# Kernel optimization log

Measured on AMD Instinct MI355X. Metric: run time of the kernel, lower is better.

Reference implementation:

```python
import jax, jax.numpy as jnp
import numpy as np

B, L, F, H, HDE, E, V, MH, MW, TOUT = 64, 2, 512, 512, 512, 512, 94, 6, 40, 30
V2 = V + 2          # vocab + START/END + NULL slots
T = TOUT + 2        # decode steps
HW = MH * MW
START = V + 1
END = V + 1


def setup_inputs() -> dict:
    key = jax.random.key(0)
    ks = jax.random.split(key, 20)
    s = 0.05  # weight scale for numerical stability
    n = lambda k, shape: jax.random.normal(k, shape, jnp.float32) * s
    d = {}
    d['conv_f'] = jax.random.normal(ks[0], (B, F, MH, MW), jnp.float32)
    d['target'] = jax.random.randint(ks[1], (B, TOUT), 0, 95, dtype=jnp.int32)
    d['w_ih_en'] = n(ks[2], (L, 4 * H, F))
    d['w_hh_en'] = n(ks[3], (L, 4 * H, H))
    d['b_ih_en'] = n(ks[4], (L, 4 * H))
    d['b_hh_en'] = n(ks[5], (L, 4 * H))
    d['embed_w'] = n(ks[6], (V2, H))
    d['w_ih_de'] = n(ks[7], (L, 4 * HDE, H))
    d['w_hh_de'] = n(ks[8], (L, 4 * HDE, HDE))
    d['b_ih_de'] = n(ks[9], (L, 4 * HDE))
    d['b_hh_de'] = n(ks[10], (L, 4 * HDE))
    d['att_wh'] = n(ks[11], (E, HDE))
    d['att_bh'] = n(ks[12], (E,))
    d['att_conv_w'] = n(ks[13], (E, F, 3, 3))
    d['att_conv_b'] = n(ks[14], (E,))
    d['att_wv'] = n(ks[15], (1, E))
    d['att_bv'] = n(ks[16], (1,))
    d['out_w'] = n(ks[17], (V2, HDE + F))
    d['out_b'] = n(ks[18], (V2,))
    return d


def _lstm_cell(x, h, c, wih, whh, bih, bhh):
    # PyTorch gate order: i, f, g, o
    g = x @ wih.T + h @ whh.T + bih + bhh
    i, f, gg, o = jnp.split(g, 4, axis=-1)
    c_new = jax.nn.sigmoid(f) * c + jax.nn.sigmoid(i) * jnp.tanh(gg)
    h_new = jax.nn.sigmoid(o) * jnp.tanh(c_new)
    return h_new, c_new


def _forward(conv_f, target, w_ih_en, w_hh_en, b_ih_en, b_hh_en, embed_w,
             w_ih_de, w_hh_de, b_ih_de, b_hh_de, att_wh, att_bh,
             att_conv_w, att_conv_b, att_wv, att_bv, out_w, out_b):
    # ---- encoder: maxpool over full height, then 2-layer LSTM over width ----
    x_seq = jnp.max(conv_f, axis=2).transpose(2, 0, 1)  # [W, B, F]

    def enc_step(carry, xt):
        h, c = carry
        inp = xt
        hs, cs = [], []
        for l in range(L):
            hl, cl = _lstm_cell(inp, h[l], c[l], w_ih_en[l], w_hh_en[l],
                                b_ih_en[l], b_hh_en[l])
            inp = hl
            hs.append(hl); cs.append(cl)
        return (jnp.stack(hs), jnp.stack(cs)), inp

    z = jnp.zeros((L, B, H), conv_f.dtype)
    _, enc_out = jax.lax.scan(enc_step, (z, z), x_seq)
    holistic = enc_out[-1]  # [B, H]

    # ---- attention: conv_f embedding computed ONCE (invariant across steps) ----
    xe = jax.lax.conv_general_dilated(
        conv_f, att_conv_w, (1, 1), 'SAME',
        dimension_numbers=('NCHW', 'OIHW', 'NCHW')) + att_conv_b[None, :, None, None]
    x_em = xe.reshape(B, E, HW).transpose(0, 2, 1)       # [B, HW, E]
    cf_flat = conv_f.reshape(B, F, HW).transpose(0, 2, 1)  # [B, HW, F]

    # ---- decoder inputs: t=0 holistic, t>=1 embed(gt_with_start[:, t-1]) ----
    gt = jnp.concatenate(
        [jnp.full((B, 1), START, dtype=target.dtype), target], axis=1)  # [B, T-1]
    xs = jnp.concatenate([holistic[None], embed_w[gt.T]], axis=0)  # [T, B, H]

    def dec_step(carry, xt):
        h, c = carry
        inp = xt
        hs, cs = [], []
        for l in range(L):
            hl, cl = _lstm_cell(inp, h[l], c[l], w_ih_de[l], w_hh_de[l],
                                b_ih_de[l], b_hh_de[l])
            inp = hl
            hs.append(hl); cs.append(cl)
        hlast = inp  # [B, HDE]
        g_em = hlast @ att_wh.T + att_bh                    # [B, E]
        feat = jnp.tanh(x_em + g_em[:, None, :])            # [B, HW, E] (dropout=identity)
        e = feat @ att_wv[0] + att_bv[0]                    # [B, HW]
        alpha = jax.nn.softmax(e, axis=-1)
        att = jnp.einsum('bw,bwf->bf', alpha, cf_flat)      # [B, F]
        logits = jnp.concatenate([hlast, att], axis=-1) @ out_w.T + out_b
        scores = jax.nn.log_softmax(logits, axis=-1)        # [B, V2]
        return (jnp.stack(hs), jnp.stack(cs)), scores

    zd = jnp.zeros((B, HDE), conv_f.dtype)
    z0 = jnp.stack([zd] * L)
    _, out_tbv = jax.lax.scan(dec_step, (z0, z0), xs)  # [T, B, V2]
    out = out_tbv.transpose(1, 0, 2)                    # [B, T, V2]

    # ---- build l_target: [0, target..., 0] with first padding 0 -> END ----
    l_target = jnp.zeros((B, T), jnp.int32).at[:, 1:-1].set(target)
    j = jnp.argmax(l_target[:, 1:] == 0, axis=1) + 1  # first zero at col>=1 (always exists)
    l_target = l_target.at[jnp.arange(B), j].set(END)

    # ---- masked NLL loss ----
    lt = l_target.reshape(-1)
    nll = -out.reshape(-1, V2)[jnp.arange(B * T), lt]
    mask = (lt != 0).astype(out.dtype)
    return jnp.sum(nll * mask) / jnp.sum(mask)


def reference(conv_f, target, w_ih_en, w_hh_en, b_ih_en, b_hh_en, embed_w,
              w_ih_de, w_hh_de, b_ih_de, b_hh_de, att_wh, att_bh,
              att_conv_w, att_conv_b, att_wv, att_bv, out_w, out_b):
    return _forward(conv_f, target, w_ih_en, w_hh_en, b_ih_en, b_hh_en, embed_w,
                    w_ih_de, w_hh_de, b_ih_de, b_hh_de, att_wh, att_bh,
                    att_conv_w, att_conv_b, att_wv, att_bv, out_w, out_b)
```

## Files before the change

### kernel.cpp

```cpp
#include <hip/hip_runtime.h>

typedef __fp16 f16;
typedef __fp16 f16x4 __attribute__((ext_vector_type(4)));
typedef __fp16 f16x8 __attribute__((ext_vector_type(8)));
typedef float  f32x4 __attribute__((ext_vector_type(4)));
typedef unsigned long long ull;

#define DEV static __device__ __forceinline__

DEV f32x4 mfma16(f16x4 a, f16x4 b, f32x4 c) {
  return __builtin_amdgcn_mfma_f32_16x16x16f16(a, b, c, 0, 0, 0);
}
DEV f16x4 lo4(f16x8 v) { return __builtin_shufflevector(v, v, 0, 1, 2, 3); }
DEV f16x4 hi4(f16x8 v) { return __builtin_shufflevector(v, v, 4, 5, 6, 7); }
DEV float sigf(float x) { return 1.f / (1.f + __expf(-x)); }
DEV float tanh_(float x) { float e = __expf(2.f * x); return 1.f - 2.f / (e + 1.f); }

union U8 { float4 f4; float2 f2[2]; };
union H2 { unsigned u; f16 h[2]; };
union H4 { ull u; f16 h[4]; f16x4 v; };

#define HB 32768

DEV ull ldU(const ull* p) {
  return __hip_atomic_load(p, __ATOMIC_RELAXED, __HIP_MEMORY_SCOPE_AGENT);
}
DEV unsigned ldF(const unsigned* p) {
  return __hip_atomic_load(p, __ATOMIC_RELAXED, __HIP_MEMORY_SCOPE_AGENT);
}
DEV void stU32(unsigned* p, unsigned v) {
  __hip_atomic_store(p, v, __ATOMIC_RELAXED, __HIP_MEMORY_SCOPE_AGENT);
}
DEV void stU64(ull* p, ull v) {
  __hip_atomic_store(p, v, __ATOMIC_RELAXED, __HIP_MEMORY_SCOPE_AGENT);
}

DEV void wait8(const unsigned* line, unsigned tgt) {
  if (threadIdx.x < 8)
    while (ldF(line + threadIdx.x * 16) < tgt) {}
  __syncthreads();
}

DEV void signalDone(unsigned* line, int slot) {
  asm volatile("s_waitcnt vmcnt(0)" ::: "memory");
  __syncthreads();
  if (threadIdx.x == 0)
    __hip_atomic_fetch_add(line + slot * 16, 1u, __ATOMIC_RELAXED, __HIP_MEMORY_SCOPE_AGENT);
}

DEV void stageRow(const f16* __restrict__ s, f16* __restrict__ dstRow, int ch) {
  U8 u0, u1;
  u0.f4 = *(const float4*)s;
  u1.f4 = *(const float4*)(s + 8);
  *(float2*)(dstRow +  0 + ch * 4) = u0.f2[0];
  *(float2*)(dstRow + 16 + ch * 4) = u0.f2[1];
  *(float2*)(dstRow + 32 + ch * 4) = u1.f2[0];
  *(float2*)(dstRow + 48 + ch * 4) = u1.f2[1];
}

DEV void stageAu(const ull* __restrict__ srcU, f16 (*A)[64][72], int tid) {
  int row = tid >> 2, ch = tid & 3;
  const ull* s = srcU + row * 128 + ch * 4;
#pragma unroll
  for (int c = 0; c < 8; ++c) {
    ull d0 = ldU(s + c * 16 + 0);
    ull d1 = ldU(s + c * 16 + 1);
    ull d2 = ldU(s + c * 16 + 2);
    ull d3 = ldU(s + c * 16 + 3);
    f16* d = &A[c][row][0];
    *(ull*)(d +  0 + ch * 4) = d0;
    *(ull*)(d + 16 + ch * 4) = d1;
    *(ull*)(d + 32 + ch * 4) = d2;
    *(ull*)(d + 48 + ch * 4) = d3;
  }
}

DEV void kloop32(const f16 (*Wt)[32][72], const f16 (*A)[64][72],
                 int mh, int ns, int m16, int g4, f32x4 acc[2]) {
#pragma unroll
  for (int c = 0; c < 8; ++c) {
#pragma unroll
    for (int half = 0; half < 2; ++half) {
      f16x8 bf = *(const f16x8*)&Wt[c][ns * 16 + m16][g4 * 16 + half * 8];
      f16x4 bl = lo4(bf), bh = hi4(bf);
#pragma unroll
      for (int mt = 0; mt < 2; ++mt) {
        f16x8 af = *(const f16x8*)&A[c][mh * 32 + mt * 16 + m16][g4 * 16 + half * 8];
        acc[mt] = mfma16(lo4(af), bl, acc[mt]);
        acc[mt] = mfma16(hi4(af), bh, acc[mt]);
      }
    }
  }
}

DEV void kloop64(const f16* Wg, const f16 (*A)[64][72],
                 int nsG, int m16, int g4, f32x4 acc[4]) {
#pragma unroll
  for (int c = 0; c < 8; ++c) {
#pragma unroll
    for (int half = 0; half < 2; ++half) {
      f16x8 bf = *(const f16x8*)&Wg[((size_t)(c * 64 + nsG * 16 + m16)) * 72 + g4 * 16 + half * 8];
      f16x4 bl = lo4(bf), bh = hi4(bf);
#pragma unroll
      for (int mt = 0; mt < 4; ++mt) {
        f16x8 af = *(const f16x8*)&A[c][mt * 16 + m16][g4 * 16 + half * 8];
        acc[mt] = mfma16(lo4(af), bl, acc[mt]);
        acc[mt] = mfma16(hi4(af), bh, acc[mt]);
      }
    }
  }
}

DEV void convTile(char* smem, int tile, const f16* __restrict__ cfT,
                  const f16* __restrict__ wc9, const float* __restrict__ cb,
                  f16* __restrict__ xemH) {
  f16 (*At)[40] = (f16(*)[40])smem;
  f16 (*Bt)[40] = (f16(*)[40])(smem + 19200);
  const int t = threadIdx.x, lane = t & 63, w = t >> 6;
  const int b = tile >> 2, eb = (tile & 3) * 128;
  const int m16 = lane & 15, g4 = lane >> 4;
  f32x4 acc[15][2] = {};

  for (int kr = 0; kr < 9; ++kr) {
    int dh = kr / 3 - 1, dw = kr % 3 - 1;
    for (int f0 = 0; f0 < 512; f0 += 32) {
      __syncthreads();
      if (t < 240) {
        int hh = t / 40 + dh, ww = t % 40 + dw;
        if (hh >= 0 && hh < 6 && ww >= 0 && ww < 40) {
          const f16* s = cfT + ((size_t)(b * 240 + hh * 40 + ww) * 512 + f0);
          U8 u0, u1, u2, u3;
          u0.f4 = *(const float4*)s;        u1.f4 = *(const float4*)(s + 8);
          u2.f4 = *(const float4*)(s + 16); u3.f4 = *(const float4*)(s + 24);
          *(float2*)&At[t][ 0] = u0.f2[0];
          *(float2*)&At[t][ 8] = u0.f2[1];
          *(float2*)&At[t][16] = u1.f2[0];
          *(float2*)&At[t][24] = u1.f2[1];
          *(float2*)&At[t][ 4] = u2.f2[0];
          *(float2*)&At[t][12] = u2.f2[1];
          *(float2*)&At[t][20] = u3.f2[0];
          *(float2*)&At[t][28] = u3.f2[1];
        } else {
          float2 z = make_float2(0.f, 0.f);
          *(float2*)&At[t][ 0] = z; *(float2*)&At[t][ 8] = z;
          *(float2*)&At[t][16] = z; *(float2*)&At[t][24] = z;
          *(float2*)&At[t][ 4] = z; *(float2*)&At[t][12] = z;
          *(float2*)&At[t][20] = z; *(float2*)&At[t][28] = z;
        }
      }
      {
        int n = t >> 1, ch = t & 1;
        const f16* s = wc9 + (size_t)(eb + n) * 4608 + kr * 512 + f0 + ch * 16;
        U8 u0, u1;
        u0.f4 = *(const float4*)s; u1.f4 = *(const float4*)(s + 8);
        *(float2*)&Bt[n][ 0 + ch * 4] = u0.f2[0];
        *(float2*)&Bt[n][ 8 + ch * 4] = u0.f2[1];
        *(float2*)&Bt[n][16 + ch * 4] = u1.f2[0];
        *(float2*)&Bt[n][24 + ch * 4] = u1.f2[1];
      }
      __syncthreads();
      f16x8 b0 = *(const f16x8*)&Bt[w * 32 + m16][g4 * 8];
      f16x8 b1v = *(const f16x8*)&Bt[w * 32 + 16 + m16][g4 * 8];
      f16x4 b0l = lo4(b0), b0h = hi4(b0), b1l = lo4(b1v), b1h = hi4(b1v);
#pragma unroll
      for (int mt = 0; mt < 15; ++mt) {
        f16x8 af = *(const f16x8*)&At[mt * 16 + m16][g4 * 8];
        f16x4 al = lo4(af), ah = hi4(af);
        acc[mt][0] = mfma16(al, b0l, acc[mt][0]);
        acc[mt][1] = mfma16(al, b1l, acc[mt][1]);
        acc[mt][0] = mfma16(ah, b0h, acc[mt][0]);
        acc[mt][1] = mfma16(ah, b1h, acc[mt][1]);
      }
    }
  }
#pragma unroll
  for (int nt = 0; nt < 2; ++nt) {
    int e = eb + w * 32 + nt * 16 + m16;
    float bias = cb[e];
#pragma unroll
    for (int mt = 0; mt < 15; ++mt)
#pragma unroll
      for (int r = 0; r < 4; ++r) {
        int p = mt * 16 + g4 * 4 + r;
        xemH[((size_t)(b * 240 + p)) * 512 + e] = (f16)(acc[mt][nt][r] + bias);
      }
  }
}


__global__ void k_convW(const float* __restrict__ s0, const float* __restrict__ s1,
                        const float* __restrict__ s2, const float* __restrict__ s3,
                        f16* __restrict__ d0, f16* __restrict__ d1,
                        f16* __restrict__ d2, f16* __restrict__ d3) {
  int i = blockIdx.x * 256 + threadIdx.x;
  int sel = i >> 19, j = i & 524287;
  const float* s = sel == 0 ? s0 : sel == 1 ? s1 : sel == 2 ? s2 : s3;
  f16* d = sel == 0 ? d0 : sel == 1 ? d1 : sel == 2 ? d2 : d3;
  float4 v = ((const float4*)s)[j];
  f16x4 o = { (f16)v.x, (f16)v.y, (f16)v.z, (f16)v.w };
  *(f16x4*)(d + (size_t)j * 4) = o;
}

__global__ void k_convS(const float* __restrict__ awhS, const float* __restrict__ embS,
                        const float* __restrict__ outwS,
                        f16* __restrict__ awhD, f16* __restrict__ embD,
                        f16* __restrict__ outwD) {
  int i = blockIdx.x * 256 + threadIdx.x;
  const float* s; f16* d; int j;
  if (i < 65536) { s = awhS; d = awhD; j = i; }
  else if (i < 65536 + 12288) { s = embS; d = embD; j = i - 65536; }
  else if (i < 65536 + 12288 + 24576) { s = outwS; d = outwD; j = i - 65536 - 12288; }
  else return;
  float4 v = ((const float4*)s)[j];
  f16x4 o = { (f16)v.x, (f16)v.y, (f16)v.z, (f16)v.w };
  *(f16x4*)(d + (size_t)j * 4) = o;
}

__global__ __launch_bounds__(256) void k_wc9(const float* __restrict__ src, f16* __restrict__ dst) {
  __shared__ float s[4608];
  const int e = blockIdx.x, tid = threadIdx.x;
  for (int i = tid; i < 4608; i += 256) s[i] = src[(size_t)e * 4608 + i];
  __syncthreads();
  for (int j = tid; j < 4608; j += 256) {
    int rr = j >> 9, f = j & 511;
    dst[(size_t)e * 4608 + j] = (f16)s[f * 9 + rr];
  }
}

__global__ __launch_bounds__(256) void k_cfmx(
    const float* __restrict__ cf, f16* __restrict__ cfT, f16* __restrict__ xseq)
{
  __shared__ float sT[64][244];
  const int tid = threadIdx.x;
  const int f0 = blockIdx.x * 64, b = blockIdx.y;
  const float* src = cf + ((size_t)b * 512 + f0) * 240;
  for (int i = tid; i < 3840; i += 256) {
    float4 v = ((const float4*)src)[i];
    int fl = i / 60, pc = (i % 60) * 4;
    sT[fl][pc] = v.x; sT[fl][pc + 1] = v.y; sT[fl][pc + 2] = v.z; sT[fl][pc + 3] = v.w;
  }
  __syncthreads();
  if (tid < 240) {
    int p = tid;
    f16* drow = cfT + ((size_t)b * 240 + p) * 512 + f0;
#pragma unroll
    for (int j = 0; j < 8; ++j) {
      f16x8 o;
#pragma unroll
      for (int k = 0; k < 8; ++k) o[k] = (f16)sT[j * 8 + k][p];
      *(f16x8*)(drow + j * 8) = o;
    }
  }
  {
    int fl = tid >> 2, wq = tid & 3;
#pragma unroll
    for (int wi = 0; wi < 10; ++wi) {
      int w = wq * 10 + wi;
      float m = sT[fl][w];
#pragma unroll
      for (int h = 1; h < 6; ++h) m = fmaxf(m, sT[fl][h * 40 + w]);
      xseq[((size_t)w * 64 + b) * 512 + f0 + fl] = (f16)m;
    }
  }
}

__global__ void k_zero(unsigned* p0, unsigned* p1, unsigned* p2,
                       unsigned* p3, unsigned* p4, unsigned* p5) {
  int i = blockIdx.x * 256 + threadIdx.x;
  int sel = i >> 14, j = i & 16383;
  unsigned* p = sel == 0 ? p0 : sel == 1 ? p1 : sel == 2 ? p2 :
                sel == 3 ? p3 : sel == 4 ? p4 : p5;
  p[j] = 0;
}

__global__ __launch_bounds__(256) void k_gemmX(
    const f16* __restrict__ A, const f16* __restrict__ W,
    const float* __restrict__ b1, const float* __restrict__ b2,
    f16* __restrict__ C)
{
  __shared__ f16 At[64][72];
  __shared__ f16 Bt[64][72];
  const int t = threadIdx.x, lane = t & 63, g = t >> 6;
  f32x4 acc[4] = {};
  const int m16 = lane & 15, g4 = lane >> 4;
  const size_t arow0 = (size_t)blockIdx.x * 64;

  for (int k0 = 0; k0 < 512; k0 += 64) {
    __syncthreads();
    { int row = t >> 2, ch = t & 3;
      stageRow(A + (arow0 + row) * 512 + k0 + ch * 16, &At[row][0], ch); }
    { int row = t >> 2, ch = t & 3;
      stageRow(W + ((size_t)blockIdx.y * 64 + row) * 512 + k0 + ch * 16, &Bt[row][0], ch); }
    __syncthreads();
#pragma unroll
    for (int half = 0; half < 2; ++half) {
      f16x8 bf = *(const f16x8*)&Bt[g * 16 + m16][g4 * 16 + half * 8];
      f16x4 bl = lo4(bf), bh = hi4(bf);
#pragma unroll
      for (int mt = 0; mt < 4; ++mt) {
        f16x8 af = *(const f16x8*)&At[mt * 16 + m16][g4 * 16 + half * 8];
        acc[mt] = mfma16(lo4(af), bl, acc[mt]);
        acc[mt] = mfma16(hi4(af), bh, acc[mt]);
      }
    }
  }
  int e = blockIdx.y * 64 + g * 16 + m16;
  float bias = b1[e] + b2[e];
#pragma unroll
  for (int mt = 0; mt < 4; ++mt)
#pragma unroll
    for (int r = 0; r < 4; ++r)
      C[(arow0 + mt * 16 + g4 * 4 + r) * 2048 + e] = (f16)(acc[mt][r] + bias);
}

__global__ __launch_bounds__(256) void k_gemmXd(
    const f16* __restrict__ x_t0, const f16* __restrict__ emb, const int* __restrict__ tgt,
    const f16* __restrict__ W, const float* __restrict__ b1, const float* __restrict__ b2,
    f16* __restrict__ C)
{
  __shared__ f16 At[64][72];
  __shared__ f16 Bt[64][72];
  const int t = threadIdx.x, lane = t & 63, g = t >> 6;
  f32x4 acc[4] = {};
  const int m16 = lane & 15, g4 = lane >> 4;
  const int tt = blockIdx.x;
  const size_t arow0 = (size_t)tt * 64;
  const int row = t >> 2, ch = t & 3;
  const f16* rowSrc;
  if (tt == 0) rowSrc = x_t0 + (size_t)row * 512;
  else if (tt == 1) rowSrc = emb + (size_t)95 * 512;
  else { int tok = tgt[row * 30 + tt - 2]; rowSrc = emb + (size_t)tok * 512; }

  for (int k0 = 0; k0 < 512; k0 += 64) {
    __syncthreads();
    stageRow(rowSrc + k0 + ch * 16, &At[row][0], ch);
    stageRow(W + ((size_t)blockIdx.y * 64 + row) * 512 + k0 + ch * 16, &Bt[row][0], ch);
    __syncthreads();
#pragma unroll
    for (int half = 0; half < 2; ++half) {
      f16x8 bf = *(const f16x8*)&Bt[g * 16 + m16][g4 * 16 + half * 8];
      f16x4 bl = lo4(bf), bh = hi4(bf);
#pragma unroll
      for (int mt = 0; mt < 4; ++mt) {
        f16x8 af = *(const f16x8*)&At[mt * 16 + m16][g4 * 16 + half * 8];
        acc[mt] = mfma16(lo4(af), bl, acc[mt]);
        acc[mt] = mfma16(hi4(af), bh, acc[mt]);
      }
    }
  }
  int e = blockIdx.y * 64 + g * 16 + m16;
  float bias = b1[e] + b2[e];
#pragma unroll
  for (int mt = 0; mt < 4; ++mt)
#pragma unroll
    for (int r = 0; r < 4; ++r)
      C[(arow0 + mt * 16 + g4 * 4 + r) * 2048 + e] = (f16)(acc[mt][r] + bias);
}

__global__ __launch_bounds__(256) void k_gemmG(
    const f16* __restrict__ A, const f16* __restrict__ W,
    const float* __restrict__ b1, f16* __restrict__ C)
{
  __shared__ f16 At[64][72];
  __shared__ f16 Bt[64][72];
  const int t = threadIdx.x, lane = t & 63, g = t >> 6;
  f32x4 acc[4] = {};
  const int m16 = lane & 15, g4 = lane >> 4;
  const size_t arow0 = (size_t)blockIdx.x * 64;

  for (int k0 = 0; k0 < 512; k0 += 64) {
    __syncthreads();
    { int row = t >> 2, ch = t & 3;
      stageRow(A + (arow0 + row) * 512 + k0 + ch * 16, &At[row][0], ch); }
    { int row = t >> 2, ch = t & 3;
      stageRow(W + ((size_t)blockIdx.y * 64 + row) * 512 + k0 + ch * 16, &Bt[row][0], ch); }
    __syncthreads();
#pragma unroll
    for (int half = 0; half < 2; ++half) {
      f16x8 bf = *(const f16x8*)&Bt[g * 16 + m16][g4 * 16 + half * 8];
      f16x4 bl = lo4(bf), bh = hi4(bf);
#pragma unroll
      for (int mt = 0; mt < 4; ++mt) {
        f16x8 af = *(const f16x8*)&At[mt * 16 + m16][g4 * 16 + half * 8];
        acc[mt] = mfma16(lo4(af), bl, acc[mt]);
        acc[mt] = mfma16(hi4(af), bh, acc[mt]);
      }
    }
  }
  int e = blockIdx.y * 64 + g * 16 + m16;
  float bias = b1[e];
#pragma unroll
  for (int mt = 0; mt < 4; ++mt)
#pragma unroll
    for (int r = 0; r < 4; ++r)
      C[(arow0 + mt * 16 + g4 * 4 + r) * 512 + e] = (f16)(acc[mt][r] + bias);
}

__global__ __launch_bounds__(256, 1) void k_lstm(
    int T,
    const f16* __restrict__ G0, const f16* __restrict__ whh0,
    const f16* __restrict__ wih1, const f16* __restrict__ whh1,
    const float* __restrict__ bih1, const float* __restrict__ bhh1,
    f16* __restrict__ h0seq, f16* __restrict__ h1seq,
    unsigned* __restrict__ cnt,
    const f16* __restrict__ cfT, const f16* __restrict__ wc9,
    const float* __restrict__ cb, f16* __restrict__ xemH, int convBase)
{
  __shared__ __align__(16) char smem[147456];
  const int tid = threadIdx.x, lane = tid & 63, w = tid >> 6;
  const int m16 = lane & 15, g4 = lane >> 4;
  const int bid = blockIdx.x;

  if (bid >= 96) {
    convTile(smem, convBase + bid - 96, cfT, wc9, cb, xemH);
    return;
  }

  if (bid < 32) {
    f16 (*sW)[64][72] = (f16(*)[64][72])smem;
    f16 (*sA)[64][72] = (f16(*)[64][72])(smem + 73728);
    float* sG = (float*)(smem + 73728);
    const int utile = bid;
    { int r = tid >> 2, ch = tid & 3;
      int grow = (r >> 4) * 512 + utile * 16 + (r & 15);
      for (int c = 0; c < 8; ++c)
        stageRow(whh0 + (size_t)grow * 512 + c * 64 + ch * 16, &sW[c][r][0], ch);
    }
    const int pb = tid >> 2, uq = tid & 3;
    float cst[4] = {0.f, 0.f, 0.f, 0.f};
    for (int t = 0; t < T; ++t) {
      if (t > 0) wait8(cnt + (size_t)(t - 1) * 128, 4);
      const f16* gpp = G0 + (size_t)(t * 64 + pb) * 2048 + utile * 16 + uq * 4;
      H4 gI, gF, gG, gO;
      gI.v = *(const f16x4*)(gpp);
      gF.v = *(const f16x4*)(gpp + 512);
      gG.v = *(const f16x4*)(gpp + 1024);
      gO.v = *(const f16x4*)(gpp + 1536);
      stageAu((const ull*)h0seq + (size_t)t * 8192, sA, tid);
      __syncthreads();
      f32x4 acc[4] = {};
      kloop64((const f16*)sW, sA, w, m16, g4, acc);
      __syncthreads();
#pragma unroll
      for (int mt = 0; mt < 4; ++mt)
#pragma unroll
        for (int r = 0; r < 4; ++r)
          sG[((size_t)w * 64 + mt * 16 + g4 * 4 + r) * 17 + m16] = acc[mt][r];
      __syncthreads();
      {
        H4 outp;
#pragma unroll
        for (int j = 0; j < 4; ++j) {
          int u = uq * 4 + j;
          float gi = sG[(0 * 64 + pb) * 17 + u] + (float)gI.h[j];
          float gf = sG[(1 * 64 + pb) * 17 + u] + (float)gF.h[j];
          float gg = sG[(2 * 64 + pb) * 17 + u] + (float)gG.h[j];
          float go = sG[(3 * 64 + pb) * 17 + u] + (float)gO.h[j];
          float cn = sigf(gf) * cst[j] + sigf(gi) * tanh_(gg);
          float hn = sigf(go) * tanh_(cn);
          cst[j] = cn;
          outp.h[j] = (f16)hn;
        }
        stU64((ull*)h0seq + (size_t)(t + 1) * 8192 + pb * 128 + utile * 4 + uq, outp.u);
      }
      signalDone(cnt + (size_t)t * 128, bid & 7);
    }
  } else {
    f16 (*sW2)[8][32][72] = (f16(*)[8][32][72])smem;
    f16 (*sA)[64][72] = (f16(*)[64][72])(smem + 73728);
    float* sG = (float*)(smem + 73728);
    const int utile = bid - 32;
    const int mh = w >> 1, ns = w & 1;
    { int mat = tid >> 7;
      int r = (tid >> 2) & 31, ch = tid & 3;
      int grow = (r >> 3) * 512 + utile * 8 + (r & 7);
      const f16* Wsrc = (mat == 0) ? wih1 : whh1;
      for (int c = 0; c < 8; ++c)
        stageRow(Wsrc + (size_t)grow * 512 + c * 64 + ch * 16, &sW2[mat][c][r][0], ch);
    }
    const int pb = tid >> 2, pup = tid & 3;
    float badd[4][2];
#pragma unroll
    for (int g = 0; g < 4; ++g)
#pragma unroll
      for (int j = 0; j < 2; ++j) {
        int rr = g * 512 + utile * 8 + pup * 2 + j;
        badd[g][j] = bih1[rr] + bhh1[rr];
      }
    float cst[2] = {0.f, 0.f};
    unsigned* line1 = cnt + (size_t)T * 128;
    for (int t = 0; t < T; ++t) {
      wait8(cnt + (size_t)t * 128, 4);
      stageAu((const ull*)h0seq + (size_t)(t + 1) * 8192, sA, tid);
      if (t > 0) wait8(line1 + (size_t)(t - 1) * 128, 8);
      else       __syncthreads();
      ull rg[8][4];
      { const ull* s1p = (const ull*)h1seq + (size_t)t * 8192 + (tid >> 2) * 128 + (tid & 3) * 4;
#pragma unroll
        for (int c = 0; c < 8; ++c)
#pragma unroll
          for (int q = 0; q < 4; ++q) rg[c][q] = ldU(s1p + c * 16 + q);
      }
      f32x4 acc[2] = {};
      kloop32(sW2[0], sA, mh, ns, m16, g4, acc);
      __syncthreads();
      { int row = tid >> 2, ch = tid & 3;
#pragma unroll
        for (int c = 0; c < 8; ++c) {
          f16* d = &sA[c][row][0];
          *(ull*)(d +  0 + ch * 4) = rg[c][0];
          *(ull*)(d + 16 + ch * 4) = rg[c][1];
          *(ull*)(d + 32 + ch * 4) = rg[c][2];
          *(ull*)(d + 48 + ch * 4) = rg[c][3];
        }
      }
      __syncthreads();
      kloop32(sW2[1], sA, mh, ns, m16, g4, acc);
      __syncthreads();
      { int nl = ns * 16 + m16;
#pragma unroll
        for (int mt = 0; mt < 2; ++mt)
#pragma unroll
          for (int r = 0; r < 4; ++r) {
            int b = mh * 32 + mt * 16 + g4 * 4 + r;
            sG[((nl >> 3) * 64 + b) * 9 + (nl & 7)] = acc[mt][r];
          }
      }
      __syncthreads();
      {
        H2 outp;
#pragma unroll
        for (int j = 0; j < 2; ++j) {
          int u = pup * 2 + j;
          float gi = sG[(0 * 64 + pb) * 9 + u] + badd[0][j];
          float gf = sG[(1 * 64 + pb) * 9 + u] + badd[1][j];
          float gg = sG[(2 * 64 + pb) * 9 + u] + badd[2][j];
          float go = sG[(3 * 64 + pb) * 9 + u] + badd[3][j];
          float cn = sigf(gf) * cst[j] + sigf(gi) * tanh_(gg);
          float hn = sigf(go) * tanh_(cn);
          cst[j] = cn;
          outp.h[j] = (f16)hn;
        }
        stU32((unsigned*)h1seq + (size_t)(t + 1) * 16384 + pb * 256 + utile * 4 + pup, outp.u);
      }
      signalDone(line1 + (size_t)t * 128, bid & 7);
    }
  }
}


__global__ __launch_bounds__(256) void k_scoreAll(
    const f16* __restrict__ xemH, const f16* __restrict__ gAll,
    const float* __restrict__ wv, float* __restrict__ esc)
{
  __shared__ f16 sX[20][512];
  const int tid = threadIdx.x, lane = tid & 63, w = tid >> 6;
  const int tile = blockIdx.x, b = blockIdx.y;
  for (int i = tid; i < 20 * 64; i += 256) {
    int row = i >> 6, seg = i & 63;
    *(f16x8*)&sX[row][seg * 8] =
        *(const f16x8*)(xemH + ((size_t)(b * 240 + tile * 20 + row)) * 512 + seg * 8);
  }
  float w8[8];
  { const float4* wp = (const float4*)(wv + lane * 8);
    float4 wa = wp[0], wb = wp[1];
    w8[0] = wa.x; w8[1] = wa.y; w8[2] = wa.z; w8[3] = wa.w;
    w8[4] = wb.x; w8[5] = wb.y; w8[6] = wb.z; w8[7] = wb.w; }
  __syncthreads();
  for (int t = 0; t < 32; ++t) {
    f16x8 gv = *(const f16x8*)(gAll + ((size_t)(t * 64 + b)) * 512 + lane * 8);
    float g8[8];
#pragma unroll
    for (int j = 0; j < 8; ++j) g8[j] = (float)gv[j];
#pragma unroll
    for (int i = 0; i < 5; ++i) {
      int rr = i * 4 + w;
      f16x8 xv = *(const f16x8*)&sX[rr][lane * 8];
      float s = 0.f;
#pragma unroll
      for (int j = 0; j < 8; ++j) s += tanh_((float)xv[j] + g8[j]) * w8[j];
#pragma unroll
      for (int m = 32; m; m >>= 1) s += __shfl_xor(s, m);
      if (lane == 0) esc[((size_t)(t * 64 + b)) * 240 + tile * 20 + rr] = s;
    }
  }
}

__global__ __launch_bounds__(256) void k_smctx(
    const float* __restrict__ esc, const f16* __restrict__ cfT,
    const f16* __restrict__ h1seq, f16* __restrict__ ctx)
{
  __shared__ float aAl[8][240];
  const int tid = threadIdx.x, lane = tid & 63, w = tid >> 6;
  const int tq = blockIdx.x, b = blockIdx.y;
  for (int half = 0; half < 2; ++half) {
    int tt = w + half * 4;
    int t = tq * 8 + tt;
    const float* er = esc + ((size_t)(t * 64 + b)) * 240;
    float v[4];
    float mx = -1e30f;
#pragma unroll
    for (int q = 0; q < 4; ++q) {
      int p = lane + q * 64;
      v[q] = (p < 240) ? er[p] : -1e30f;
      mx = fmaxf(mx, v[q]);
    }
#pragma unroll
    for (int m = 32; m; m >>= 1) mx = fmaxf(mx, __shfl_xor(mx, m));
    float sum = 0.f;
#pragma unroll
    for (int q = 0; q < 4; ++q) { v[q] = __expf(v[q] - mx); sum += v[q]; }
#pragma unroll
    for (int m = 32; m; m >>= 1) sum += __shfl_xor(sum, m);
    float inv = 1.f / sum;
#pragma unroll
    for (int q = 0; q < 4; ++q) {
      int p = lane + q * 64;
      if (p < 240) aAl[tt][p] = v[q] * inv;
    }
  }
  __syncthreads();
  float acc[8][2] = {};
  const f16* cb = cfT + (size_t)b * 240 * 512;
  for (int p = 0; p < 240; ++p) {
    H2 cw; cw.u = *(const unsigned*)(cb + (size_t)p * 512 + tid * 2);
    float c0 = (float)cw.h[0], c1 = (float)cw.h[1];
#pragma unroll
    for (int tt = 0; tt < 8; ++tt) {
      float a = aAl[tt][p];
      acc[tt][0] += a * c0;
      acc[tt][1] += a * c1;
    }
  }
#pragma unroll
  for (int tt = 0; tt < 8; ++tt) {
    int t = tq * 8 + tt;
    size_t r = (size_t)(t * 64 + b);
    H2 o; o.h[0] = (f16)acc[tt][0]; o.h[1] = (f16)acc[tt][1];
    *(unsigned*)(ctx + r * 1024 + 512 + tid * 2) = o.u;
    *(unsigned*)(ctx + r * 1024 + tid * 2) =
        *(const unsigned*)(h1seq + (size_t)(t + 1) * HB + b * 512 + tid * 2);
  }
}

__global__ __launch_bounds__(256) void k_gemmL(
    const f16* __restrict__ A, const f16* __restrict__ W,
    const float* __restrict__ bias, float* __restrict__ C)
{
  __shared__ f16 At[64][72];
  __shared__ f16 Bt[64][72];
  const int t = threadIdx.x, lane = t & 63, g = t >> 6;
  f32x4 acc[4] = {};
  const int m16 = lane & 15, g4 = lane >> 4;
  const size_t arow0 = (size_t)blockIdx.x * 64;

  for (int k0 = 0; k0 < 1024; k0 += 64) {
    __syncthreads();
    { int row = t >> 2, ch = t & 3;
      stageRow(A + (arow0 + row) * 1024 + k0 + ch * 16, &At[row][0], ch); }
    { int row = t >> 2, ch = t & 3;
      stageRow(W + ((size_t)(blockIdx.y * 64 + row)) * 1024 + k0 + ch * 16, &Bt[row][0], ch); }
    __syncthreads();
#pragma unroll
    for (int half = 0; half < 2; ++half) {
      f16x8 bf = *(const f16x8*)&Bt[g * 16 + m16][g4 * 16 + half * 8];
      f16x4 bl = lo4(bf), bh = hi4(bf);
#pragma unroll
      for (int mt = 0; mt < 4; ++mt) {
        f16x8 af = *(const f16x8*)&At[mt * 16 + m16][g4 * 16 + half * 8];
        acc[mt] = mfma16(lo4(af), bl, acc[mt]);
        acc[mt] = mfma16(hi4(af), bh, acc[mt]);
      }
    }
  }
  int e = blockIdx.y * 64 + g * 16 + m16;
  if (e < 96) {
    float be = bias[e];
#pragma unroll
    for (int mt = 0; mt < 4; ++mt)
#pragma unroll
      for (int r = 0; r < 4; ++r)
        C[(arow0 + mt * 16 + g4 * 4 + r) * 96 + e] = acc[mt][r] + be;
  }
}

__global__ void k_nllloss(const float* __restrict__ lgt, const int* __restrict__ target,
                          float* __restrict__ out) {
  __shared__ int ltg[2048];
  __shared__ float sa[256], sb[256];
  int tid = threadIdx.x;
  if (tid < 64) {
    int b = tid;
    int row[32];
    row[0] = 0;
    for (int t = 1; t <= 30; ++t) row[t] = target[b * 30 + t - 1];
    row[31] = 0;
    int j = 1;
    while (row[j] != 0) ++j;
    row[j] = 95;
    for (int t = 0; t < 32; ++t) ltg[b * 32 + t] = row[t];
  }
  __syncthreads();
  float a = 0.f, m = 0.f;
  for (int r = tid; r < 2048; r += 256) {
    int t = r >> 6, b = r & 63;
    int tok = ltg[b * 32 + t];
    if (tok != 0) {
      const float* row = lgt + (size_t)r * 96;
      float mx = -1e30f;
      for (int j = 0; j < 96; ++j) mx = fmaxf(mx, row[j]);
      float s = 0.f;
      for (int j = 0; j < 96; ++j) s += __expf(row[j] - mx);
      a += mx + __logf(s) - row[tok];
      m += 1.f;
    }
  }
  sa[tid] = a; sb[tid] = m; __syncthreads();
  for (int s = 128; s; s >>= 1) { if (tid < s) { sa[tid] += sa[tid + s]; sb[tid] += sb[tid + s]; } __syncthreads(); }
  if (tid == 0) out[0] = sa[0] / sb[0];
}


extern "C" void kernel_launch(void* const* d_in, const int* in_sizes, int n_in,
                              void* d_out, int out_size, void* d_ws, size_t ws_size,
                              hipStream_t stream) {
  (void)in_sizes; (void)n_in; (void)out_size; (void)ws_size;
  const float* conv_f = (const float*)d_in[0];
  const int*   target = (const int*)d_in[1];
  const float* wih_en = (const float*)d_in[2];
  const float* whh_en = (const float*)d_in[3];
  const float* bih_en = (const float*)d_in[4];
  const float* bhh_en = (const float*)d_in[5];
  const float* embed  = (const float*)d_in[6];
  const float* wih_de = (const float*)d_in[7];
  const float* whh_de = (const float*)d_in[8];
  const float* bih_de = (const float*)d_in[9];
  const float* bhh_de = (const float*)d_in[10];
  const float* att_wh = (const float*)d_in[11];
  const float* att_bh = (const float*)d_in[12];
  const float* att_cw = (const float*)d_in[13];
  const float* att_cb = (const float*)d_in[14];
  const float* att_wv = (const float*)d_in[15];
  const float* out_w  = (const float*)d_in[17];
  const float* out_b  = (const float*)d_in[18];
  float* out = (float*)d_out;

  size_t o = 0;
  char* base = (char*)d_ws;
  auto take = [&](size_t bytes) -> void* {
    void* p = base + o;
    o += (bytes + 255) & ~(size_t)255;
    return p;
  };
  const size_t WSZ = (size_t)2048 * 512;
  f16* wihEn = (f16*)take(2 * WSZ * 2);
  f16* whhEn = (f16*)take(2 * WSZ * 2);
  f16* wihDe = (f16*)take(2 * WSZ * 2);
  f16* whhDe = (f16*)take(2 * WSZ * 2);
  f16* awh   = (f16*)take((size_t)512 * 512 * 2);
  f16* emb   = (f16*)take((size_t)96 * 512 * 2);
  f16* wc9   = (f16*)take((size_t)512 * 4608 * 2);
  f16* cfT   = (f16*)take((size_t)64 * 240 * 512 * 2);
  f16* xseq  = (f16*)take((size_t)40 * 64 * 512 * 2);
  f16* xemH  = (f16*)take((size_t)64 * 240 * 512 * 2);
  f16* outwH = (f16*)take((size_t)128 * 1024 * 2);
  f16* X0en  = (f16*)take((size_t)2560 * 2048 * 2);
  f16* X0de  = (f16*)take((size_t)2048 * 2048 * 2);
  f16* h0seqE = (f16*)take((size_t)41 * HB * 2);
  f16* h1seqE = (f16*)take((size_t)41 * HB * 2);
  f16* h0seqD = (f16*)take((size_t)33 * HB * 2);
  f16* h1seqD = (f16*)take((size_t)33 * HB * 2);
  f16* gAll   = (f16*)take((size_t)2048 * 512 * 2);
  unsigned* cntE = (unsigned*)take(65536);
  unsigned* cntD = (unsigned*)take(65536);
  float* escAll = (float*)X0en;
  float* lgtAll = (float*)((char*)X0en + 4194304);
  f16*   ctxAll = X0de;

  k_convW<<<8192, 256, 0, stream>>>(wih_en, whh_en, wih_de, whh_de,
                                    wihEn, whhEn, wihDe, whhDe);
  k_convS<<<400, 256, 0, stream>>>(att_wh, embed, out_w, awh, emb, outwH);
  k_wc9<<<512, 256, 0, stream>>>(att_cw, wc9);
  k_cfmx<<<dim3(8, 64), 256, 0, stream>>>(conv_f, cfT, xseq);
  k_zero<<<384, 256, 0, stream>>>((unsigned*)h0seqE, (unsigned*)h1seqE,
                                  (unsigned*)h0seqD, (unsigned*)h1seqD, cntE, cntD);

  k_gemmX<<<dim3(40, 32), 256, 0, stream>>>(xseq, wihEn, bih_en, bhh_en, X0en);
  k_lstm<<<224, 256, 0, stream>>>(40, X0en, whhEn, wihEn + WSZ, whhEn + WSZ,
                                  bih_en + 2048, bhh_en + 2048, h0seqE, h1seqE, cntE,
                                  cfT, wc9, att_cb, xemH, 0);

  k_gemmXd<<<dim3(32, 32), 256, 0, stream>>>(h1seqE + (size_t)40 * HB, emb, target,
                                             wihDe, bih_de, bhh_de, X0de);
  k_lstm<<<224, 256, 0, stream>>>(32, X0de, whhDe, wihDe + WSZ, whhDe + WSZ,
                                  bih_de + 2048, bhh_de + 2048, h0seqD, h1seqD, cntD,
                                  cfT, wc9, att_cb, xemH, 128);

  k_gemmG<<<dim3(32, 8), 256, 0, stream>>>(h1seqD + HB, awh, att_bh, gAll);
  k_scoreAll<<<dim3(12, 64), 256, 0, stream>>>(xemH, gAll, att_wv, escAll);
  k_smctx<<<dim3(4, 64), 256, 0, stream>>>(escAll, cfT, h1seqD, ctxAll);
  k_gemmL<<<dim3(32, 2), 256, 0, stream>>>(ctxAll, outwH, out_b, lgtAll);
  k_nllloss<<<1, 256, 0, stream>>>(lgtAll, target, out);
}
```

Before: 856.4 us.

## Fold decoder input GEMM and attention projection GEMM into persistent LSTM kernels

The encoder LSTM launch gains 32 extra blocks that compute the decoder layer-0 input projection for steps 1..31 from the embeddings while the encoder recurrence runs. The separate decoder input GEMM is cut down to the one step that depends on the final encoder state. The decoder LSTM launch gains 8 blocks that poll the layer-1 step counters and compute the attention hidden projection (gAll) per step as each h1 becomes ready, replacing the separate k_gemmG launch. This overlaps otherwise serial GEMMs with the latency-bound recurrence, but it adds co-resident blocks that spin-wait and assumes all 256 or 232 blocks are resident at once.

```diff
diff --git a/kernel.cpp b/kernel.cpp
--- a/kernel.cpp
+++ b/kernel.cpp
@@ -56,6 +56,14 @@
   *(float2*)(dstRow + 16 + ch * 4) = u0.f2[1];
   *(float2*)(dstRow + 32 + ch * 4) = u1.f2[0];
   *(float2*)(dstRow + 48 + ch * 4) = u1.f2[1];
+}
+
+DEV void stageAp(const f16* __restrict__ rowSrc, f16 (*A)[64][72], int tid) {
+  int ch = tid & 3;
+  const f16* s = rowSrc + ch * 16;
+#pragma unroll
+  for (int c = 0; c < 8; ++c)
+    stageRow(s + c * 64, &A[c][tid >> 2][0], ch);
 }
 
 DEV void stageAu(const ull* __restrict__ srcU, f16 (*A)[64][72], int tid) {
@@ -357,64 +365,24 @@
       C[(arow0 + mt * 16 + g4 * 4 + r) * 2048 + e] = (f16)(acc[mt][r] + bias);
 }
 
-__global__ __launch_bounds__(256) void k_gemmG(
-    const f16* __restrict__ A, const f16* __restrict__ W,
-    const float* __restrict__ b1, f16* __restrict__ C)
-{
-  __shared__ f16 At[64][72];
-  __shared__ f16 Bt[64][72];
-  const int t = threadIdx.x, lane = t & 63, g = t >> 6;
-  f32x4 acc[4] = {};
-  const int m16 = lane & 15, g4 = lane >> 4;
-  const size_t arow0 = (size_t)blockIdx.x * 64;
-
-  for (int k0 = 0; k0 < 512; k0 += 64) {
-    __syncthreads();
-    { int row = t >> 2, ch = t & 3;
-      stageRow(A + (arow0 + row) * 512 + k0 + ch * 16, &At[row][0], ch); }
-    { int row = t >> 2, ch = t & 3;
-      stageRow(W + ((size_t)blockIdx.y * 64 + row) * 512 + k0 + ch * 16, &Bt[row][0], ch); }
-    __syncthreads();
-#pragma unroll
-    for (int half = 0; half < 2; ++half) {
-      f16x8 bf = *(const f16x8*)&Bt[g * 16 + m16][g4 * 16 + half * 8];
-      f16x4 bl = lo4(bf), bh = hi4(bf);
-#pragma unroll
-      for (int mt = 0; mt < 4; ++mt) {
-        f16x8 af = *(const f16x8*)&At[mt * 16 + m16][g4 * 16 + half * 8];
-        acc[mt] = mfma16(lo4(af), bl, acc[mt]);
-        acc[mt] = mfma16(hi4(af), bh, acc[mt]);
-      }
-    }
-  }
-  int e = blockIdx.y * 64 + g * 16 + m16;
-  float bias = b1[e];
-#pragma unroll
-  for (int mt = 0; mt < 4; ++mt)
-#pragma unroll
-    for (int r = 0; r < 4; ++r)
-      C[(arow0 + mt * 16 + g4 * 4 + r) * 512 + e] = (f16)(acc[mt][r] + bias);
-}
-
 __global__ __launch_bounds__(256, 1) void k_lstm(
-    int T,
+    int T, int mode,
     const f16* __restrict__ G0, const f16* __restrict__ whh0,
     const f16* __restrict__ wih1, const f16* __restrict__ whh1,
     const float* __restrict__ bih1, const float* __restrict__ bhh1,
     f16* __restrict__ h0seq, f16* __restrict__ h1seq,
     unsigned* __restrict__ cnt,
     const f16* __restrict__ cfT, const f16* __restrict__ wc9,
-    const float* __restrict__ cb, f16* __restrict__ xemH, int convBase)
+    const float* __restrict__ cb, f16* __restrict__ xemH, int convBase,
+    f16* __restrict__ X0de, const f16* __restrict__ wihD0,
+    const float* __restrict__ bihD0, const float* __restrict__ bhhD0,
+    const f16* __restrict__ emb, const int* __restrict__ tgt,
+    const f16* __restrict__ awh, const float* __restrict__ gbias, f16* __restrict__ gAll)
 {
   __shared__ __align__(16) char smem[147456];
   const int tid = threadIdx.x, lane = tid & 63, w = tid >> 6;
   const int m16 = lane & 15, g4 = lane >> 4;
   const int bid = blockIdx.x;
-
-  if (bid >= 96) {
-    convTile(smem, convBase + bid - 96, cfT, wc9, cb, xemH);
-    return;
-  }
 
   if (bid < 32) {
     f16 (*sW)[64][72] = (f16(*)[64][72])smem;
@@ -465,7 +433,7 @@
       }
       signalDone(cnt + (size_t)t * 128, bid & 7);
     }
-  } else {
+  } else if (bid < 96) {
     f16 (*sW2)[8][32][72] = (f16(*)[8][32][72])smem;
     f16 (*sA)[64][72] = (f16(*)[64][72])(smem + 73728);
     float* sG = (float*)(smem + 73728);
@@ -544,6 +512,61 @@
         stU32((unsigned*)h1seq + (size_t)(t + 1) * 16384 + pb * 256 + utile * 4 + pup, outp.u);
       }
       signalDone(line1 + (size_t)t * 128, bid & 7);
+    }
+  } else if (bid < 224) {
+    convTile(smem, convBase + bid - 96, cfT, wc9, cb, xemH);
+  } else if (mode == 0) {
+    const int rid = bid - 224;
+    f16 (*sW)[64][72] = (f16(*)[64][72])smem;
+    f16 (*sA)[64][72] = (f16(*)[64][72])(smem + 73728);
+    { int r = tid >> 2, ch = tid & 3;
+      for (int c = 0; c < 8; ++c)
+        stageRow(wihD0 + (size_t)(rid * 64 + r) * 512 + c * 64 + ch * 16, &sW[c][r][0], ch);
+    }
+    const int e = rid * 64 + w * 16 + m16;
+    const float bias_e = bihD0[e] + bhhD0[e];
+    const int arow = tid >> 2;
+    __syncthreads();
+    for (int tt = 1; tt < 32; ++tt) {
+      const f16* rowSrc = (tt == 1) ? emb + (size_t)95 * 512
+                                    : emb + (size_t)tgt[arow * 30 + tt - 2] * 512;
+      stageAp(rowSrc, sA, tid);
+      __syncthreads();
+      f32x4 acc[4] = {};
+      kloop64((const f16*)sW, sA, w, m16, g4, acc);
+      __syncthreads();
+#pragma unroll
+      for (int mt = 0; mt < 4; ++mt)
+#pragma unroll
+        for (int r = 0; r < 4; ++r)
+          X0de[((size_t)tt * 64 + mt * 16 + g4 * 4 + r) * 2048 + e] = (f16)(acc[mt][r] + bias_e);
+      __syncthreads();
+    }
+  } else {
+    const int g = bid - 224;
+    f16* sWg = (f16*)smem;
+    f16 (*sA)[64][72] = (f16(*)[64][72])(smem + 73728);
+    { int r = tid >> 2, ch = tid & 3;
+      for (int c = 0; c < 8; ++c)
+        stageRow(awh + (size_t)(g * 64 + r) * 512 + c * 64 + ch * 16,
+                 sWg + ((size_t)(c * 64 + r)) * 72, ch);
+    }
+    const int e = g * 64 + w * 16 + m16;
+    const float gb = gbias[e];
+    __syncthreads();
+    unsigned* line1 = cnt + (size_t)T * 128;
+    for (int t = 0; t < T; ++t) {
+      wait8(line1 + (size_t)t * 128, 8);
+      stageAu((const ull*)h1seq + (size_t)(t + 1) * 8192, sA, tid);
+      __syncthreads();
+      f32x4 acc[4] = {};
+      kloop64(sWg, sA, w, m16, g4, acc);
+      __syncthreads();
+#pragma unroll
+      for (int mt = 0; mt < 4; ++mt)
+#pragma unroll
+        for (int r = 0; r < 4; ++r)
+          gAll[(size_t)(t * 64 + mt * 16 + g4 * 4 + r) * 512 + e] = (f16)(acc[mt][r] + gb);
     }
   }
 }
@@ -786,17 +809,20 @@
                                   (unsigned*)h0seqD, (unsigned*)h1seqD, cntE, cntD);
 
   k_gemmX<<<dim3(40, 32), 256, 0, stream>>>(xseq, wihEn, bih_en, bhh_en, X0en);
-  k_lstm<<<224, 256, 0, stream>>>(40, X0en, whhEn, wihEn + WSZ, whhEn + WSZ,
+  k_lstm<<<256, 256, 0, stream>>>(40, 0, X0en, whhEn, wihEn + WSZ, whhEn + WSZ,
                                   bih_en + 2048, bhh_en + 2048, h0seqE, h1seqE, cntE,
-                                  cfT, wc9, att_cb, xemH, 0);
-
-  k_gemmXd<<<dim3(32, 32), 256, 0, stream>>>(h1seqE + (size_t)40 * HB, emb, target,
-                                             wihDe, bih_de, bhh_de, X0de);
-  k_lstm<<<224, 256, 0, stream>>>(32, X0de, whhDe, wihDe + WSZ, whhDe + WSZ,
+                                  cfT, wc9, att_cb, xemH, 0,
+                                  X0de, wihDe, bih_de, bhh_de, emb, target,
+                                  nullptr, nullptr, nullptr);
+
+  k_gemmXd<<<dim3(1, 32), 256, 0, stream>>>(h1seqE + (size_t)40 * HB, emb, target,
+                                            wihDe, bih_de, bhh_de, X0de);
+  k_lstm<<<232, 256, 0, stream>>>(32, 1, X0de, whhDe, wihDe + WSZ, whhDe + WSZ,
                                   bih_de + 2048, bhh_de + 2048, h0seqD, h1seqD, cntD,
-                                  cfT, wc9, att_cb, xemH, 128);
-
-  k_gemmG<<<dim3(32, 8), 256, 0, stream>>>(h1seqD + HB, awh, att_bh, gAll);
+                                  cfT, wc9, att_cb, xemH, 128,
+                                  nullptr, nullptr, nullptr, nullptr, emb, target,
+                                  awh, att_bh, gAll);
+
   k_scoreAll<<<dim3(12, 64), 256, 0, stream>>>(xemH, gAll, att_wv, escAll);
   k_smctx<<<dim3(4, 64), 256, 0, stream>>>(escAll, cfT, h1seqD, ctxAll);
   k_gemmL<<<dim3(32, 2), 256, 0, stream>>>(ctxAll, outwH, out_b, lgtAll);
```

After: 849.7 us. Within noise of the previous version (-0.8%).
